# Performance work log

Measured on AMD Instinct MI355X. Metric: run time of the kernel, lower is better.

Reference implementation:

```python
import jax, jax.numpy as jnp
import numpy as np

B, S, F = 32, 8, 4
N0, N1, N2 = 2048, 4096, 2048
H, OUT = 1024, 256
IN = N0 + N1 + N2  # 8192
SC_LAYERS = 2


def setup_inputs() -> dict:
    key = jax.random.key(0)
    ks = jax.random.split(key, 16)
    rn = jax.random.normal
    inp = {
        'xs0': rn(ks[0], (B, S, N0), jnp.float32),
        'xs1': rn(ks[1], (B, S, N1), jnp.float32),
        'xs2': rn(ks[2], (B, S, N2), jnp.float32),
        # dense Laplacians, scaled so L@x keeps unit-ish variance
        'L0': rn(ks[3], (N0, N0), jnp.float32) / np.sqrt(N0).astype(np.float32),
        'L1': rn(ks[4], (N1, N1), jnp.float32) / np.sqrt(N1).astype(np.float32),
        'L2': rn(ks[5], (N2, N2), jnp.float32) / np.sqrt(N2).astype(np.float32),
        # per-layer, per-filter diagonal weights (std=0.01 as in torch init)
        'Wc0': 0.01 * rn(ks[6], (SC_LAYERS, F, N0), jnp.float32),
        'Wc1': 0.01 * rn(ks[7], (SC_LAYERS, F, N1), jnp.float32),
        'Wc2': 0.01 * rn(ks[8], (SC_LAYERS, F, N2), jnp.float32),
        # MLP params (xavier-ish)
        'W_in': rn(ks[9], (IN, H), jnp.float32) / np.sqrt(IN).astype(np.float32),
        'b_in': jnp.zeros((H,), jnp.float32),
        'W_h': rn(ks[10], (H, H), jnp.float32) / np.sqrt(H).astype(np.float32),
        'b_h': jnp.zeros((H,), jnp.float32),
        'W_out': rn(ks[11], (H, OUT), jnp.float32) / np.sqrt(H).astype(np.float32),
        'b_out': jnp.zeros((OUT,), jnp.float32),
    }
    return inp


def _conv_stack(x, L, Wc):
    # x: [B, S, n]; L: [n, n]; Wc: [layers, F, n]
    for l in range(Wc.shape[0]):
        # batched Laplacian matmul: (L @ x_bs) for every (b, s)
        Lx = jnp.einsum('bsn,mn->bsm', x, L)  # [B, S, n]
        # diagonal filter scaling + activation + sum over filters (fused)
        x = jax.nn.relu(Lx[:, :, None, :] * Wc[l][None, None, :, :]).sum(axis=2)
    return x


def reference(xs0, xs1, xs2, L0, L1, L2, Wc0, Wc1, Wc2,
              W_in, b_in, W_h, b_h, W_out, b_out):
    h = jnp.concatenate([
        _conv_stack(xs0, L0, Wc0),
        _conv_stack(xs1, L1, Wc1),
        _conv_stack(xs2, L2, Wc2),
    ], axis=-1)                      # [B, S, IN]
    h = h.sum(axis=1)                # sum over sequence -> [B, IN]
    h = jax.nn.relu(h @ W_in + b_in)
    h = jax.nn.relu(h @ W_h + b_h)   # single hidden layer (nn_layers=2)
    return h @ W_out + b_out         # [B, OUT]
```

## Files before the change

### kernel.cpp

```cpp
#include <hip/hip_runtime.h>
#include <hip/hip_bf16.h>


#define B_    32
#define S_    8
#define BS_   256
#define F_    4
#define IN_   8192
#define H_    1024
#define OUT_  256

#define L_TOT  25165824LL
#define LOFF1  4194304LL
#define LOFF2  20971520LL

typedef __attribute__((ext_vector_type(8)))  short bf16x8;
typedef __attribute__((ext_vector_type(4)))  short short4v;
typedef __attribute__((ext_vector_type(16))) float f32x16;

typedef const __attribute__((address_space(1))) void* gas_ptr;
typedef __attribute__((address_space(3))) void* las_ptr;

__device__ __forceinline__ void gload16(const void* g, void* s) {
    __builtin_amdgcn_global_load_lds((gas_ptr)g, (las_ptr)s, 16, 0, 0);
}

__device__ __forceinline__ unsigned short rne_bf16(float f) {
    unsigned int u = __builtin_bit_cast(unsigned int, f);
    u += 0x7FFFu + ((u >> 16) & 1u);
    return (unsigned short)(u >> 16);
}

__global__ void k_prep(const float* __restrict__ Wc0, const float* __restrict__ Wc1,
                       const float* __restrict__ Wc2, float* __restrict__ PM) {
    int idx = blockIdx.x * 256 + threadIdx.x;
    if (idx >= 2 * IN_) return;
    int l = idx / IN_, n = idx % IN_;
    const float* Wc; int nb, j;
    if (n < 2048)      { Wc = Wc0; nb = 2048; j = n;        }
    else if (n < 6144) { Wc = Wc1; nb = 4096; j = n - 2048; }
    else               { Wc = Wc2; nb = 2048; j = n - 6144; }
    float p = 0.f, m = 0.f;
    #pragma unroll
    for (int f = 0; f < F_; ++f) {
        float w = Wc[(l * F_ + f) * nb + j];
        p += fmaxf(w, 0.f);
        m += fmaxf(-w, 0.f);
    }
    PM[(l * 2 + 0) * IN_ + n] = p;
    PM[(l * 2 + 1) * IN_ + n] = m;
}

__global__ void k_cvtL(const float* __restrict__ L0, const float* __restrict__ L1,
                       const float* __restrict__ L2, unsigned short* __restrict__ Lb) {
    long long e = ((long long)blockIdx.x * 256 + threadIdx.x) * 4;
    if (e >= L_TOT) return;
    const float* src; long long off;
    if (e < LOFF1)      { src = L0; off = 0; }
    else if (e < LOFF2) { src = L1; off = LOFF1; }
    else                { src = L2; off = LOFF2; }
    float4 v = *(const float4*)(src + (e - off));
    short4v o;
    o.x = (short)rne_bf16(v.x); o.y = (short)rne_bf16(v.y);
    o.z = (short)rne_bf16(v.z); o.w = (short)rne_bf16(v.w);
    *(short4v*)(Lb + e) = o;
}

__global__ void k_splitX(const float* __restrict__ x0, const float* __restrict__ x1,
                         const float* __restrict__ x2,
                         unsigned short* __restrict__ Xhi, unsigned short* __restrict__ Xlo) {
    int e = (blockIdx.x * 256 + threadIdx.x) * 4;
    int m = e >> 13, c = e & 8191;
    const float* src; int n, c0;
    if (c < 2048)      { src = x0; n = 2048; c0 = c; }
    else if (c < 6144) { src = x1; n = 4096; c0 = c - 2048; }
    else               { src = x2; n = 2048; c0 = c - 6144; }
    float4 v = *(const float4*)(src + (size_t)m * n + c0);
    float a[4] = {v.x, v.y, v.z, v.w};
    short hv[4], lv[4];
    #pragma unroll
    for (int i = 0; i < 4; ++i) {
        unsigned short hb = rne_bf16(a[i]);
        float hf = __builtin_bit_cast(float, (unsigned int)hb << 16);
        hv[i] = (short)hb;
        lv[i] = (short)rne_bf16(a[i] - hf);
    }
    short4v h = {hv[0], hv[1], hv[2], hv[3]};
    short4v l = {lv[0], lv[1], lv[2], lv[3]};
    *(short4v*)(Xhi + (size_t)m * IN_ + c) = h;
    *(short4v*)(Xlo + (size_t)m * IN_ + c) = l;
}

__global__ __launch_bounds__(256, 2) void k_gemm(
    const unsigned short* __restrict__ Astk,
    const unsigned short* __restrict__ Lb,
    float* __restrict__ pf)
{
    __shared__ __attribute__((aligned(16))) unsigned short ldsA[2][128 * 64];
    __shared__ __attribute__((aligned(16))) unsigned short ldsB[2][128 * 64];

    const int bx = blockIdx.x;
    const int sk = bx & 1, t = bx >> 1;
    int n_, noff, mt, nt; long long loff;
    if (t < 64)       { mt = t >> 4;         nt = t & 15;        n_ = 2048; noff = 0;    loff = 0;     }
    else if (t < 192) { int u = t - 64;  mt = u >> 5; nt = u & 31; n_ = 4096; noff = 2048; loff = LOFF1; }
    else              { int u = t - 192; mt = u >> 4; nt = u & 15; n_ = 2048; noff = 6144; loff = LOFF2; }

    const int tid = threadIdx.x, l = tid & 63, w = tid >> 6;
    const int n2 = n_ >> 1, k0 = sk * n2, iters = n2 >> 6;

    const int srow = w * 32 + (l >> 3);
    const int cswz = ((l & 7) ^ (l >> 3)) << 3;
    const unsigned short* gA = Astk + (size_t)(mt * 128 + srow) * IN_ + noff + k0 + cswz;
    const unsigned short* gB = Lb + loff + (size_t)(nt * 128 + srow) * n_ + k0 + cswz;

    const int l31 = l & 31, lh = l >> 5, l7 = l31 & 7;
    const int wm = w >> 1, wn = w & 1;
    const int arow = (wm * 64 + l31) * 64;
    const int brow = (wn * 64 + l31) * 64;

    f32x16 a00, a01, a10, a11;
    #pragma unroll
    for (int r = 0; r < 16; ++r) { a00[r] = 0.f; a01[r] = 0.f; a10[r] = 0.f; a11[r] = 0.f; }

    #pragma unroll
    for (int q = 0; q < 4; ++q) {
        gload16(gA + (size_t)q * 8 * IN_, &ldsA[0][(w * 32 + q * 8) * 64]);
        gload16(gB + (size_t)q * 8 * n_, &ldsB[0][(w * 32 + q * 8) * 64]);
    }
    __syncthreads();

    for (int it = 0; it < iters; ++it) {
        const unsigned short* La = (it & 1) ? &ldsA[1][0] : &ldsA[0][0];
        const unsigned short* Bb = (it & 1) ? &ldsB[1][0] : &ldsB[0][0];
        unsigned short* Sa = (it & 1) ? &ldsA[0][0] : &ldsA[1][0];
        unsigned short* Sb = (it & 1) ? &ldsB[0][0] : &ldsB[1][0];

        if (it + 1 < iters) {
            const int kofs = (it + 1) * 64;
            #pragma unroll
            for (int q = 0; q < 4; ++q) {
                gload16(gA + (size_t)q * 8 * IN_ + kofs, Sa + (w * 32 + q * 8) * 64);
                gload16(gB + (size_t)q * 8 * n_ + kofs, Sb + (w * 32 + q * 8) * 64);
            }
        }

        #pragma unroll
        for (int t2 = 0; t2 < 4; ++t2) {
            const int xs = (((t2 * 2 + lh) ^ l7) << 3);
            bf16x8 fa0 = *(const bf16x8*)&La[arow + xs];
            bf16x8 fa1 = *(const bf16x8*)&La[arow + 32 * 64 + xs];
            bf16x8 fb0 = *(const bf16x8*)&Bb[brow + xs];
            bf16x8 fb1 = *(const bf16x8*)&Bb[brow + 32 * 64 + xs];
            a00 = __builtin_amdgcn_mfma_f32_32x32x16_bf16(fa0, fb0, a00, 0, 0, 0);
            a01 = __builtin_amdgcn_mfma_f32_32x32x16_bf16(fa0, fb1, a01, 0, 0, 0);
            a10 = __builtin_amdgcn_mfma_f32_32x32x16_bf16(fa1, fb0, a10, 0, 0, 0);
            a11 = __builtin_amdgcn_mfma_f32_32x32x16_bf16(fa1, fb1, a11, 0, 0, 0);
        }
        __syncthreads();
    }

    const int gcolb = noff + nt * 128 + wn * 64 + l31;
    float* po = pf + ((size_t)sk * 512 + (size_t)mt * 128 + wm * 64 + 4 * lh) * IN_;
    #pragma unroll
    for (int r = 0; r < 16; ++r) {
        int row = (r & 3) + 8 * (r >> 2);
        po[(size_t)row * IN_ + gcolb]           = a00[r];
        po[(size_t)row * IN_ + gcolb + 32]      = a01[r];
        po[(size_t)(row + 32) * IN_ + gcolb]    = a10[r];
        po[(size_t)(row + 32) * IN_ + gcolb+32] = a11[r];
    }
}

template<int LAYER>
__global__ void k_epi(const float* __restrict__ pf,
                      const float* __restrict__ Pv, const float* __restrict__ Mv,
                      unsigned short* __restrict__ Yhi, unsigned short* __restrict__ Ylo,
                      float* __restrict__ Yf) {
    int e = (blockIdx.x * 256 + threadIdx.x) * 4;
    int m = e >> 13, c = e & 8191;
    const float* p0 = pf + (size_t)m * IN_ + c;
    float4 vh0 = *(const float4*)(p0);
    float4 vl0 = *(const float4*)(p0 + (size_t)256 * IN_);
    float4 vh1 = *(const float4*)(p0 + (size_t)512 * IN_);
    float4 vl1 = *(const float4*)(p0 + (size_t)768 * IN_);
    float4 pv = *(const float4*)(Pv + c);
    float4 mv = *(const float4*)(Mv + c);
    float vs[4] = {vh0.x + vl0.x + vh1.x + vl1.x, vh0.y + vl0.y + vh1.y + vl1.y,
                   vh0.z + vl0.z + vh1.z + vl1.z, vh0.w + vl0.w + vh1.w + vl1.w};
    float pa[4] = {pv.x, pv.y, pv.z, pv.w};
    float ma[4] = {mv.x, mv.y, mv.z, mv.w};
    if (LAYER == 0) {
        short hv[4], lv[4];
        #pragma unroll
        for (int j = 0; j < 4; ++j) {
            float y = fmaxf(vs[j], 0.f) * pa[j] + fmaxf(-vs[j], 0.f) * ma[j];
            unsigned short hb = rne_bf16(y);
            float hf = __builtin_bit_cast(float, (unsigned int)hb << 16);
            hv[j] = (short)hb;
            lv[j] = (short)rne_bf16(y - hf);
        }
        short4v h = {hv[0], hv[1], hv[2], hv[3]};
        short4v lo = {lv[0], lv[1], lv[2], lv[3]};
        *(short4v*)(Yhi + (size_t)m * IN_ + c) = h;
        *(short4v*)(Ylo + (size_t)m * IN_ + c) = lo;
    } else {
        float ov[4];
        #pragma unroll
        for (int j = 0; j < 4; ++j)
            ov[j] = fmaxf(vs[j], 0.f) * pa[j] + fmaxf(-vs[j], 0.f) * ma[j];
        *(float4*)(Yf + (size_t)m * IN_ + c) = *(float4*)ov;
    }
}

__global__ void k_sums(const float* __restrict__ X, float* __restrict__ Y) {
    int idx = blockIdx.x * 256 + threadIdx.x;
    int b = idx >> 13, n = idx & 8191;
    const float* p = X + (size_t)b * 8 * IN_ + n;
    float s = 0.f;
    #pragma unroll
    for (int q = 0; q < 8; ++q) s += p[(size_t)q * IN_];
    Y[idx] = s;
}

template<int KC>
__global__ __launch_bounds__(256) void k_mlp3(
    const float* __restrict__ X, const float* __restrict__ W,
    float* __restrict__ P, int K, int H)
{
    __shared__ float Xs[32][KC];
    const int tid = threadIdx.x;
    const int lane = tid & 63;
    const int mg = tid >> 6;
    const int h = (blockIdx.x * 64 + lane) * 4;
    const int c = blockIdx.y, k0 = c * KC;

    for (int i = tid * 4; i < 32 * KC; i += 1024) {
        int m = i / KC, kk = i % KC;
        *(float4*)&Xs[m][kk] = *(const float4*)(X + (size_t)m * K + k0 + kk);
    }
    __syncthreads();

    float4 acc[8];
    #pragma unroll
    for (int m = 0; m < 8; ++m) acc[m] = {0.f, 0.f, 0.f, 0.f};

    const float* wp = W + (size_t)k0 * H + h;
    for (int kk = 0; kk < KC; kk += 4) {
        float4 w4[4];
        #pragma unroll
        for (int u = 0; u < 4; ++u)
            w4[u] = *(const float4*)(wp + (size_t)(kk + u) * H);
        #pragma unroll
        for (int m = 0; m < 8; ++m) {
            float4 xv = *(const float4*)&Xs[mg * 8 + m][kk];
            acc[m].x = fmaf(xv.x, w4[0].x, acc[m].x);
            acc[m].y = fmaf(xv.x, w4[0].y, acc[m].y);
            acc[m].z = fmaf(xv.x, w4[0].z, acc[m].z);
            acc[m].w = fmaf(xv.x, w4[0].w, acc[m].w);
            acc[m].x = fmaf(xv.y, w4[1].x, acc[m].x);
            acc[m].y = fmaf(xv.y, w4[1].y, acc[m].y);
            acc[m].z = fmaf(xv.y, w4[1].z, acc[m].z);
            acc[m].w = fmaf(xv.y, w4[1].w, acc[m].w);
            acc[m].x = fmaf(xv.z, w4[2].x, acc[m].x);
            acc[m].y = fmaf(xv.z, w4[2].y, acc[m].y);
            acc[m].z = fmaf(xv.z, w4[2].z, acc[m].z);
            acc[m].w = fmaf(xv.z, w4[2].w, acc[m].w);
            acc[m].x = fmaf(xv.w, w4[3].x, acc[m].x);
            acc[m].y = fmaf(xv.w, w4[3].y, acc[m].y);
            acc[m].z = fmaf(xv.w, w4[3].z, acc[m].z);
            acc[m].w = fmaf(xv.w, w4[3].w, acc[m].w);
        }
    }
    #pragma unroll
    for (int m = 0; m < 8; ++m)
        *(float4*)(P + ((size_t)c * 32 + mg * 8 + m) * H + h) = acc[m];
}

__global__ void k_reduce4(const float* __restrict__ P, const float* __restrict__ bias,
                          float* __restrict__ Y, int NC, int MH4, int H, int do_relu) {
    int idx = blockIdx.x * 256 + threadIdx.x;
    if (idx >= MH4) return;
    int h0 = (idx * 4) % H;
    float4 s = *(const float4*)(bias + h0);
    for (int c = 0; c < NC; ++c) {
        float4 v = *(const float4*)(P + (size_t)c * MH4 * 4 + (size_t)idx * 4);
        s.x += v.x; s.y += v.y; s.z += v.z; s.w += v.w;
    }
    if (do_relu) {
        s.x = fmaxf(s.x, 0.f); s.y = fmaxf(s.y, 0.f);
        s.z = fmaxf(s.z, 0.f); s.w = fmaxf(s.w, 0.f);
    }
    *(float4*)(Y + (size_t)idx * 4) = s;
}

extern "C" void kernel_launch(void* const* d_in, const int* in_sizes, int n_in,
                              void* d_out, int out_size, void* d_ws, size_t ws_size,
                              hipStream_t stream) {
    const float* xs0  = (const float*)d_in[0];
    const float* xs1  = (const float*)d_in[1];
    const float* xs2  = (const float*)d_in[2];
    const float* L0   = (const float*)d_in[3];
    const float* L1   = (const float*)d_in[4];
    const float* L2   = (const float*)d_in[5];
    const float* Wc0  = (const float*)d_in[6];
    const float* Wc1  = (const float*)d_in[7];
    const float* Wc2  = (const float*)d_in[8];
    const float* W_in = (const float*)d_in[9];
    const float* b_in = (const float*)d_in[10];
    const float* W_h  = (const float*)d_in[11];
    const float* b_h  = (const float*)d_in[12];
    const float* W_out= (const float*)d_in[13];
    const float* b_out= (const float*)d_in[14];

    char* w = (char*)d_ws;
    float*          PM = (float*)w;           w += (size_t)4 * IN_ * 4;
    unsigned short* Lb = (unsigned short*)w;  w += (size_t)L_TOT * 2;
    unsigned short* Xs = (unsigned short*)w;  w += (size_t)512 * IN_ * 2;
    unsigned short* Ys = (unsigned short*)w;  w += (size_t)512 * IN_ * 2;
    float*          pf = (float*)w;           w += (size_t)2 * 512 * IN_ * 4;
    float*          xB = (float*)Xs;
    float*          hsum = (float*)w;         w += (size_t)32 * IN_ * 4;
    float*          p1 = pf;
    float*          h1 = (float*)w;           w += (size_t)32 * H_ * 4;
    float*          p2 = (float*)w;           w += (size_t)32 * 32 * H_ * 4;
    float*          h2 = (float*)w;           w += (size_t)32 * H_ * 4;
    float*          p3 = (float*)w;           w += (size_t)32 * 32 * OUT_ * 4;

    k_prep<<<64, 256, 0, stream>>>(Wc0, Wc1, Wc2, PM);
    k_cvtL<<<24576, 256, 0, stream>>>(L0, L1, L2, Lb);
    k_splitX<<<2048, 256, 0, stream>>>(xs0, xs1, xs2, Xs, Xs + (size_t)256 * IN_);

    k_gemm<<<512, 256, 0, stream>>>(Xs, Lb, pf);
    k_epi<0><<<2048, 256, 0, stream>>>(pf, PM + 0 * IN_, PM + 1 * IN_,
                                       Ys, Ys + (size_t)256 * IN_, nullptr);
    k_gemm<<<512, 256, 0, stream>>>(Ys, Lb, pf);
    k_epi<1><<<2048, 256, 0, stream>>>(pf, PM + 2 * IN_, PM + 3 * IN_,
                                       nullptr, nullptr, xB);

    k_sums<<<1024, 256, 0, stream>>>(xB, hsum);

    {
        dim3 g(4, 128);
        k_mlp3<64><<<g, 256, 0, stream>>>(hsum, W_in, p1, IN_, H_);
        k_reduce4<<<32, 256, 0, stream>>>(p1, b_in, h1, 128, 8192, H_, 1);
    }
    {
        dim3 g(4, 32);
        k_mlp3<32><<<g, 256, 0, stream>>>(h1, W_h, p2, H_, H_);
        k_reduce4<<<32, 256, 0, stream>>>(p2, b_h, h2, 32, 8192, H_, 1);
    }
    {
        dim3 g(1, 32);
        k_mlp3<32><<<g, 256, 0, stream>>>(h2, W_out, p3, H_, OUT_);
        k_reduce4<<<8, 256, 0, stream>>>(p3, b_out, (float*)d_out, 32, 2048, OUT_, 0);
    }
}
```

Baseline: 209.3 us.

## Restructure Laplacian GEMM to fuse hi/lo split into MFMA and fuse epilogue with sequence sum

The GEMM no longer stacks the hi and lo bf16 halves of X as separate M rows. Instead each block loads both halves and issues two MFMAs against the same L fragment, so every L tile is read once for both halves. Tiles shrink to 64x128 with K-step 32, and the K-split becomes 4 for the 4096 block, giving 768 blocks at 3 waves per SIMD. The layer-1 epilogue is fused with the sequence sum, k_cvtL becomes a grid-stride loop, and the epilogue reduces a variable number of K-split partials. The cost is more partial-sum traffic for the large block and smaller K-steps with more barriers.

```diff
diff --git a/kernel.cpp b/kernel.cpp
--- a/kernel.cpp
+++ b/kernel.cpp
@@ -53,17 +53,20 @@
 
 __global__ void k_cvtL(const float* __restrict__ L0, const float* __restrict__ L1,
                        const float* __restrict__ L2, unsigned short* __restrict__ Lb) {
-    long long e = ((long long)blockIdx.x * 256 + threadIdx.x) * 4;
-    if (e >= L_TOT) return;
-    const float* src; long long off;
-    if (e < LOFF1)      { src = L0; off = 0; }
-    else if (e < LOFF2) { src = L1; off = LOFF1; }
-    else                { src = L2; off = LOFF2; }
-    float4 v = *(const float4*)(src + (e - off));
-    short4v o;
-    o.x = (short)rne_bf16(v.x); o.y = (short)rne_bf16(v.y);
-    o.z = (short)rne_bf16(v.z); o.w = (short)rne_bf16(v.w);
-    *(short4v*)(Lb + e) = o;
+    const int gid = blockIdx.x * 256 + threadIdx.x;
+    #pragma unroll 4
+    for (int it = 0; it < 12; ++it) {
+        long long e = ((long long)it * 524288 + gid) * 4;
+        const float* src; long long off;
+        if (e < LOFF1)      { src = L0; off = 0; }
+        else if (e < LOFF2) { src = L1; off = LOFF1; }
+        else                { src = L2; off = LOFF2; }
+        float4 v = *(const float4*)(src + (e - off));
+        short4v o;
+        o.x = (short)rne_bf16(v.x); o.y = (short)rne_bf16(v.y);
+        o.z = (short)rne_bf16(v.z); o.w = (short)rne_bf16(v.w);
+        *(short4v*)(Lb + e) = o;
+    }
 }
 
 __global__ void k_splitX(const float* __restrict__ x0, const float* __restrict__ x1,
@@ -91,136 +94,144 @@
     *(short4v*)(Xlo + (size_t)m * IN_ + c) = l;
 }
 
-__global__ __launch_bounds__(256, 2) void k_gemm(
-    const unsigned short* __restrict__ Astk,
+__global__ __launch_bounds__(256, 3) void k_gemm(
+    const unsigned short* __restrict__ Xhi, const unsigned short* __restrict__ Xlo,
     const unsigned short* __restrict__ Lb,
     float* __restrict__ pf)
 {
-    __shared__ __attribute__((aligned(16))) unsigned short ldsA[2][128 * 64];
-    __shared__ __attribute__((aligned(16))) unsigned short ldsB[2][128 * 64];
+    __shared__ __attribute__((aligned(16))) unsigned short Ah[2][64 * 32];
+    __shared__ __attribute__((aligned(16))) unsigned short Al[2][64 * 32];
+    __shared__ __attribute__((aligned(16))) unsigned short Bs[2][128 * 32];
 
     const int bx = blockIdx.x;
-    const int sk = bx & 1, t = bx >> 1;
-    int n_, noff, mt, nt; long long loff;
-    if (t < 64)       { mt = t >> 4;         nt = t & 15;        n_ = 2048; noff = 0;    loff = 0;     }
-    else if (t < 192) { int u = t - 64;  mt = u >> 5; nt = u & 31; n_ = 4096; noff = 2048; loff = LOFF1; }
-    else              { int u = t - 192; mt = u >> 4; nt = u & 15; n_ = 2048; noff = 6144; loff = LOFF2; }
+    int n_, noff, mt, nt, sk; long long loff;
+    if (bx < 128) {
+        int u = bx; sk = u & 1; u >>= 1; mt = u >> 4; nt = u & 15;
+        n_ = 2048; noff = 0; loff = 0;
+    } else if (bx < 640) {
+        int u = bx - 128; sk = u & 3; u >>= 2; mt = u >> 5; nt = u & 31;
+        n_ = 4096; noff = 2048; loff = LOFF1;
+    } else {
+        int u = bx - 640; sk = u & 1; u >>= 1; mt = u >> 4; nt = u & 15;
+        n_ = 2048; noff = 6144; loff = LOFF2;
+    }
+    const int k0 = sk << 10;
 
     const int tid = threadIdx.x, l = tid & 63, w = tid >> 6;
-    const int n2 = n_ >> 1, k0 = sk * n2, iters = n2 >> 6;
-
-    const int srow = w * 32 + (l >> 3);
-    const int cswz = ((l & 7) ^ (l >> 3)) << 3;
-    const unsigned short* gA = Astk + (size_t)(mt * 128 + srow) * IN_ + noff + k0 + cswz;
-    const unsigned short* gB = Lb + loff + (size_t)(nt * 128 + srow) * n_ + k0 + cswz;
-
-    const int l31 = l & 31, lh = l >> 5, l7 = l31 & 7;
+
+    const int sr  = 16 * w + (l >> 2);
+    const int slg = (((l & 3) ^ ((l >> 3) & 3)) << 3);
+    const unsigned short* gAh = Xhi + (size_t)(mt * 64 + sr) * IN_ + noff + k0 + slg;
+    const unsigned short* gAl = Xlo + (size_t)(mt * 64 + sr) * IN_ + noff + k0 + slg;
+    const unsigned short* gB0 = Lb + loff + (size_t)(nt * 128 + sr) * n_ + k0 + slg;
+    const unsigned short* gB1 = Lb + loff + (size_t)(nt * 128 + 64 + sr) * n_ + k0 + slg;
+    char* dAh[2] = {(char*)&Ah[0][0] + w * 1024, (char*)&Ah[1][0] + w * 1024};
+    char* dAl[2] = {(char*)&Al[0][0] + w * 1024, (char*)&Al[1][0] + w * 1024};
+    char* dB0[2] = {(char*)&Bs[0][0] + w * 1024, (char*)&Bs[1][0] + w * 1024};
+    char* dB1[2] = {(char*)&Bs[0][0] + 4096 + w * 1024, (char*)&Bs[1][0] + 4096 + w * 1024};
+
+    const int l31 = l & 31, lh = l >> 5;
     const int wm = w >> 1, wn = w & 1;
-    const int arow = (wm * 64 + l31) * 64;
-    const int brow = (wn * 64 + l31) * 64;
-
-    f32x16 a00, a01, a10, a11;
-    #pragma unroll
-    for (int r = 0; r < 16; ++r) { a00[r] = 0.f; a01[r] = 0.f; a10[r] = 0.f; a11[r] = 0.f; }
-
-    #pragma unroll
-    for (int q = 0; q < 4; ++q) {
-        gload16(gA + (size_t)q * 8 * IN_, &ldsA[0][(w * 32 + q * 8) * 64]);
-        gload16(gB + (size_t)q * 8 * n_, &ldsB[0][(w * 32 + q * 8) * 64]);
-    }
+    const int ra  = (wm * 32 + l31) * 32;
+    const int rb0 = (wn * 64 + l31) * 32;
+    const int rb1 = rb0 + 32 * 32;
+    const int swz = ((l31 >> 1) & 3);
+
+    f32x16 acc0, acc1;
+    #pragma unroll
+    for (int r = 0; r < 16; ++r) { acc0[r] = 0.f; acc1[r] = 0.f; }
+
+    gload16(gAh, dAh[0]); gload16(gAl, dAl[0]);
+    gload16(gB0, dB0[0]); gload16(gB1, dB1[0]);
     __syncthreads();
 
-    for (int it = 0; it < iters; ++it) {
-        const unsigned short* La = (it & 1) ? &ldsA[1][0] : &ldsA[0][0];
-        const unsigned short* Bb = (it & 1) ? &ldsB[1][0] : &ldsB[0][0];
-        unsigned short* Sa = (it & 1) ? &ldsA[0][0] : &ldsA[1][0];
-        unsigned short* Sb = (it & 1) ? &ldsB[0][0] : &ldsB[1][0];
-
-        if (it + 1 < iters) {
-            const int kofs = (it + 1) * 64;
-            #pragma unroll
-            for (int q = 0; q < 4; ++q) {
-                gload16(gA + (size_t)q * 8 * IN_ + kofs, Sa + (w * 32 + q * 8) * 64);
-                gload16(gB + (size_t)q * 8 * n_ + kofs, Sb + (w * 32 + q * 8) * 64);
-            }
+    for (int it = 0; it < 32; ++it) {
+        const int cur = it & 1, nxt = cur ^ 1;
+        if (it + 1 < 32) {
+            const int ko = (it + 1) * 32;
+            gload16(gAh + ko, dAh[nxt]); gload16(gAl + ko, dAl[nxt]);
+            gload16(gB0 + ko, dB0[nxt]); gload16(gB1 + ko, dB1[nxt]);
         }
-
         #pragma unroll
-        for (int t2 = 0; t2 < 4; ++t2) {
-            const int xs = (((t2 * 2 + lh) ^ l7) << 3);
-            bf16x8 fa0 = *(const bf16x8*)&La[arow + xs];
-            bf16x8 fa1 = *(const bf16x8*)&La[arow + 32 * 64 + xs];
-            bf16x8 fb0 = *(const bf16x8*)&Bb[brow + xs];
-            bf16x8 fb1 = *(const bf16x8*)&Bb[brow + 32 * 64 + xs];
-            a00 = __builtin_amdgcn_mfma_f32_32x32x16_bf16(fa0, fb0, a00, 0, 0, 0);
-            a01 = __builtin_amdgcn_mfma_f32_32x32x16_bf16(fa0, fb1, a01, 0, 0, 0);
-            a10 = __builtin_amdgcn_mfma_f32_32x32x16_bf16(fa1, fb0, a10, 0, 0, 0);
-            a11 = __builtin_amdgcn_mfma_f32_32x32x16_bf16(fa1, fb1, a11, 0, 0, 0);
+        for (int t = 0; t < 2; ++t) {
+            const int sidx = (((2 * t + lh) ^ swz) << 3);
+            bf16x8 fah = *(const bf16x8*)&Ah[cur][ra + sidx];
+            bf16x8 fal = *(const bf16x8*)&Al[cur][ra + sidx];
+            bf16x8 fb0 = *(const bf16x8*)&Bs[cur][rb0 + sidx];
+            bf16x8 fb1 = *(const bf16x8*)&Bs[cur][rb1 + sidx];
+            acc0 = __builtin_amdgcn_mfma_f32_32x32x16_bf16(fal, fb0, acc0, 0, 0, 0);
+            acc0 = __builtin_amdgcn_mfma_f32_32x32x16_bf16(fah, fb0, acc0, 0, 0, 0);
+            acc1 = __builtin_amdgcn_mfma_f32_32x32x16_bf16(fal, fb1, acc1, 0, 0, 0);
+            acc1 = __builtin_amdgcn_mfma_f32_32x32x16_bf16(fah, fb1, acc1, 0, 0, 0);
         }
         __syncthreads();
     }
 
-    const int gcolb = noff + nt * 128 + wn * 64 + l31;
-    float* po = pf + ((size_t)sk * 512 + (size_t)mt * 128 + wm * 64 + 4 * lh) * IN_;
+    const int colg = noff + nt * 128 + wn * 64 + l31;
+    float* po = pf + ((size_t)sk * 256 + (size_t)mt * 64 + wm * 32 + 4 * lh) * IN_;
     #pragma unroll
     for (int r = 0; r < 16; ++r) {
         int row = (r & 3) + 8 * (r >> 2);
-        po[(size_t)row * IN_ + gcolb]           = a00[r];
-        po[(size_t)row * IN_ + gcolb + 32]      = a01[r];
-        po[(size_t)(row + 32) * IN_ + gcolb]    = a10[r];
-        po[(size_t)(row + 32) * IN_ + gcolb+32] = a11[r];
-    }
-}
-
-template<int LAYER>
-__global__ void k_epi(const float* __restrict__ pf,
-                      const float* __restrict__ Pv, const float* __restrict__ Mv,
-                      unsigned short* __restrict__ Yhi, unsigned short* __restrict__ Ylo,
-                      float* __restrict__ Yf) {
+        po[(size_t)row * IN_ + colg]      = acc0[r];
+        po[(size_t)row * IN_ + colg + 32] = acc1[r];
+    }
+}
+
+__global__ void k_epi0(const float* __restrict__ pf,
+                       const float* __restrict__ Pv, const float* __restrict__ Mv,
+                       unsigned short* __restrict__ Yhi, unsigned short* __restrict__ Ylo) {
     int e = (blockIdx.x * 256 + threadIdx.x) * 4;
     int m = e >> 13, c = e & 8191;
+    const int nsl = (c >= 2048 && c < 6144) ? 4 : 2;
     const float* p0 = pf + (size_t)m * IN_ + c;
-    float4 vh0 = *(const float4*)(p0);
-    float4 vl0 = *(const float4*)(p0 + (size_t)256 * IN_);
-    float4 vh1 = *(const float4*)(p0 + (size_t)512 * IN_);
-    float4 vl1 = *(const float4*)(p0 + (size_t)768 * IN_);
+    float vs[4] = {0.f, 0.f, 0.f, 0.f};
+    for (int s = 0; s < nsl; ++s) {
+        float4 v = *(const float4*)(p0 + (size_t)s * 256 * IN_);
+        vs[0] += v.x; vs[1] += v.y; vs[2] += v.z; vs[3] += v.w;
+    }
     float4 pv = *(const float4*)(Pv + c);
     float4 mv = *(const float4*)(Mv + c);
-    float vs[4] = {vh0.x + vl0.x + vh1.x + vl1.x, vh0.y + vl0.y + vh1.y + vl1.y,
-                   vh0.z + vl0.z + vh1.z + vl1.z, vh0.w + vl0.w + vh1.w + vl1.w};
     float pa[4] = {pv.x, pv.y, pv.z, pv.w};
     float ma[4] = {mv.x, mv.y, mv.z, mv.w};
-    if (LAYER == 0) {
-        short hv[4], lv[4];
-        #pragma unroll
-        for (int j = 0; j < 4; ++j) {
-            float y = fmaxf(vs[j], 0.f) * pa[j] + fmaxf(-vs[j], 0.f) * ma[j];
-            unsigned short hb = rne_bf16(y);
-            float hf = __builtin_bit_cast(float, (unsigned int)hb << 16);
-            hv[j] = (short)hb;
-            lv[j] = (short)rne_bf16(y - hf);
+    short hv[4], lv[4];
+    #pragma unroll
+    for (int j = 0; j < 4; ++j) {
+        float y = fmaxf(vs[j], 0.f) * pa[j] + fmaxf(-vs[j], 0.f) * ma[j];
+        unsigned short hb = rne_bf16(y);
+        float hf = __builtin_bit_cast(float, (unsigned int)hb << 16);
+        hv[j] = (short)hb;
+        lv[j] = (short)rne_bf16(y - hf);
+    }
+    short4v h = {hv[0], hv[1], hv[2], hv[3]};
+    short4v lo = {lv[0], lv[1], lv[2], lv[3]};
+    *(short4v*)(Yhi + (size_t)m * IN_ + c) = h;
+    *(short4v*)(Ylo + (size_t)m * IN_ + c) = lo;
+}
+
+__global__ void k_epi1s(const float* __restrict__ pf,
+                        const float* __restrict__ Pv, const float* __restrict__ Mv,
+                        float* __restrict__ hsum) {
+    int e = (blockIdx.x * 256 + threadIdx.x) * 4;
+    int b = e >> 13, c = e & 8191;
+    const int nsl = (c >= 2048 && c < 6144) ? 4 : 2;
+    float4 pv = *(const float4*)(Pv + c);
+    float4 mv = *(const float4*)(Mv + c);
+    float pa[4] = {pv.x, pv.y, pv.z, pv.w};
+    float ma[4] = {mv.x, mv.y, mv.z, mv.w};
+    float hs[4] = {0.f, 0.f, 0.f, 0.f};
+    for (int q = 0; q < 8; ++q) {
+        const int m = b * 8 + q;
+        const float* p0 = pf + (size_t)m * IN_ + c;
+        float vs[4] = {0.f, 0.f, 0.f, 0.f};
+        for (int s = 0; s < nsl; ++s) {
+            float4 v = *(const float4*)(p0 + (size_t)s * 256 * IN_);
+            vs[0] += v.x; vs[1] += v.y; vs[2] += v.z; vs[3] += v.w;
         }
-        short4v h = {hv[0], hv[1], hv[2], hv[3]};
-        short4v lo = {lv[0], lv[1], lv[2], lv[3]};
-        *(short4v*)(Yhi + (size_t)m * IN_ + c) = h;
-        *(short4v*)(Ylo + (size_t)m * IN_ + c) = lo;
-    } else {
-        float ov[4];
         #pragma unroll
         for (int j = 0; j < 4; ++j)
-            ov[j] = fmaxf(vs[j], 0.f) * pa[j] + fmaxf(-vs[j], 0.f) * ma[j];
-        *(float4*)(Yf + (size_t)m * IN_ + c) = *(float4*)ov;
-    }
-}
-
-__global__ void k_sums(const float* __restrict__ X, float* __restrict__ Y) {
-    int idx = blockIdx.x * 256 + threadIdx.x;
-    int b = idx >> 13, n = idx & 8191;
-    const float* p = X + (size_t)b * 8 * IN_ + n;
-    float s = 0.f;
-    #pragma unroll
-    for (int q = 0; q < 8; ++q) s += p[(size_t)q * IN_];
-    Y[idx] = s;
+            hs[j] += fmaxf(vs[j], 0.f) * pa[j] + fmaxf(-vs[j], 0.f) * ma[j];
+    }
+    *(float4*)(hsum + (size_t)b * IN_ + c) = *(float4*)hs;
 }
 
 template<int KC>
@@ -314,31 +325,28 @@
     const float* b_out= (const float*)d_in[14];
 
     char* w = (char*)d_ws;
-    float*          PM = (float*)w;           w += (size_t)4 * IN_ * 4;
-    unsigned short* Lb = (unsigned short*)w;  w += (size_t)L_TOT * 2;
-    unsigned short* Xs = (unsigned short*)w;  w += (size_t)512 * IN_ * 2;
-    unsigned short* Ys = (unsigned short*)w;  w += (size_t)512 * IN_ * 2;
-    float*          pf = (float*)w;           w += (size_t)2 * 512 * IN_ * 4;
-    float*          xB = (float*)Xs;
-    float*          hsum = (float*)w;         w += (size_t)32 * IN_ * 4;
-    float*          p1 = pf;
-    float*          h1 = (float*)w;           w += (size_t)32 * H_ * 4;
-    float*          p2 = (float*)w;           w += (size_t)32 * 32 * H_ * 4;
-    float*          h2 = (float*)w;           w += (size_t)32 * H_ * 4;
-    float*          p3 = (float*)w;           w += (size_t)32 * 32 * OUT_ * 4;
+    float*          PM  = (float*)w;          w += (size_t)4 * IN_ * 4;
+    unsigned short* Lb  = (unsigned short*)w; w += (size_t)L_TOT * 2;
+    unsigned short* Xhi = (unsigned short*)w; w += (size_t)BS_ * IN_ * 2;
+    unsigned short* Xlo = (unsigned short*)w; w += (size_t)BS_ * IN_ * 2;
+    unsigned short* Yhi = (unsigned short*)w; w += (size_t)BS_ * IN_ * 2;
+    unsigned short* Ylo = (unsigned short*)w; w += (size_t)BS_ * IN_ * 2;
+    float*          pf  = (float*)w;          w += (size_t)4 * BS_ * IN_ * 4;
+    float*          hsum= (float*)w;          w += (size_t)32 * IN_ * 4;
+    float*          p1  = pf;
+    float*          h1  = (float*)w;          w += (size_t)32 * H_ * 4;
+    float*          p2  = (float*)w;          w += (size_t)32 * 32 * H_ * 4;
+    float*          h2  = (float*)w;          w += (size_t)32 * H_ * 4;
+    float*          p3  = (float*)w;          w += (size_t)32 * 32 * OUT_ * 4;
 
     k_prep<<<64, 256, 0, stream>>>(Wc0, Wc1, Wc2, PM);
-    k_cvtL<<<24576, 256, 0, stream>>>(L0, L1, L2, Lb);
-    k_splitX<<<2048, 256, 0, stream>>>(xs0, xs1, xs2, Xs, Xs + (size_t)256 * IN_);
-
-    k_gemm<<<512, 256, 0, stream>>>(Xs, Lb, pf);
-    k_epi<0><<<2048, 256, 0, stream>>>(pf, PM + 0 * IN_, PM + 1 * IN_,
-                                       Ys, Ys + (size_t)256 * IN_, nullptr);
-    k_gemm<<<512, 256, 0, stream>>>(Ys, Lb, pf);
-    k_epi<1><<<2048, 256, 0, stream>>>(pf, PM + 2 * IN_, PM + 3 * IN_,
-                                       nullptr, nullptr, xB);
-
-    k_sums<<<1024, 256, 0, stream>>>(xB, hsum);
+    k_cvtL<<<2048, 256, 0, stream>>>(L0, L1, L2, Lb);
+    k_splitX<<<2048, 256, 0, stream>>>(xs0, xs1, xs2, Xhi, Xlo);
+
+    k_gemm<<<768, 256, 0, stream>>>(Xhi, Xlo, Lb, pf);
+    k_epi0<<<2048, 256, 0, stream>>>(pf, PM + 0 * IN_, PM + 1 * IN_, Yhi, Ylo);
+    k_gemm<<<768, 256, 0, stream>>>(Yhi, Ylo, Lb, pf);
+    k_epi1s<<<256, 256, 0, stream>>>(pf, PM + 2 * IN_, PM + 3 * IN_, hsum);
 
     {
         dim3 g(4, 128);
```

Measured after the change: 211.9 us. About the same (+1.2%).
